# Kernel optimization log

Hardware: AMD Instinct MI355X
Metric: run time of the kernel (lower is better)

## Reference

```python
import math
import jax, jax.numpy as jnp
import numpy as np

B, S, HID, NH = 8, 512, 1024, 16
D = HID // NH          # head dim = 64
SPAN = 512             # att_span = max_relative_positions = max_position_embeddings


def _linear(x, W, b):
    # torch nn.Linear: y = x @ W.T + b, W is [out, in]
    return jnp.einsum('...i,oi->...o', x, W) + b


def _heads(x):
    # [B, S, HID] -> [B, NH, S, D]
    b, s, _ = x.shape
    return x.reshape(b, s, NH, D).transpose(0, 2, 1, 3)


def setup_inputs() -> dict:
    key = jax.random.key(0)
    ks = jax.random.split(key, 16)
    f = lambda i, shape, sc=1.0: jax.random.normal(ks[i], shape, dtype=jnp.float32) * sc
    return {
        'q': f(0, (B, S, HID)),
        'k': f(1, (B, S, HID)),
        'v': f(2, (B, S, HID)),
        'attention_mask': jnp.tril(jnp.ones((S, S), dtype=bool))[None, None],  # causal [1,1,S,S]
        'Wq': f(3, (HID, HID), 0.02), 'bq': jnp.zeros((HID,), jnp.float32),
        'Wk': f(4, (HID, HID), 0.02), 'bk': jnp.zeros((HID,), jnp.float32),
        'Wv': f(5, (HID, HID), 0.02), 'bv': jnp.zeros((HID,), jnp.float32),
        'Wpk': f(6, (HID, HID), 0.02), 'bpk': jnp.zeros((HID,), jnp.float32),
        'Wpq': f(7, (HID, HID), 0.02), 'bpq': jnp.zeros((HID,), jnp.float32),
        'rel_emb': f(8, (2 * SPAN, HID), 0.02),
    }


def reference(q, k, v, attention_mask, Wq, bq, Wk, bk, Wv, bv, Wpk, bpk, Wpq, bpq, rel_emb):
    scale_factor = 3  # 1 (content) + c2p + p2c
    scale = 1.0 / math.sqrt(D * scale_factor)

    ql = _heads(_linear(q, Wq, bq))   # [B,NH,S,D]
    kl = _heads(_linear(k, Wk, bk))
    vl = _heads(_linear(v, Wv, bv))

    # content-to-content scores
    scores = jnp.einsum('bhqd,bhkd->bhqk', ql, kl) * scale

    # relative positions (no bucketing since position_buckets = -1)
    rel = jnp.arange(S)[:, None] - jnp.arange(S)[None, :]          # [S,S]
    c2p_pos = jnp.clip(rel + SPAN, 0, 2 * SPAN - 1)
    p2c_pos = jnp.clip(-rel + SPAN, 0, 2 * SPAN - 1)

    # projected relative-position embeddings -> [NH, 2*SPAN, D]
    pk = _linear(rel_emb, Wpk, bpk).reshape(2 * SPAN, NH, D).transpose(1, 0, 2)
    pq = _linear(rel_emb, Wpq, bpq).reshape(2 * SPAN, NH, D).transpose(1, 0, 2)

    # content-to-position: out[b,h,q,k] = (q . pos_key)[b,h,q, c2p_pos[q,k]]
    c2p = jnp.einsum('bhqd,hjd->bhqj', ql, pk) * scale             # [B,NH,S,2*SPAN]
    c2p = jnp.take_along_axis(c2p, jnp.broadcast_to(c2p_pos[None, None], (B, NH, S, S)), axis=-1)

    # position-to-content: gathered[b,h,k,q] = (k . pos_query)[b,h,k, p2c_pos[k,q]], then transpose
    p2c = jnp.einsum('bhkd,hjd->bhkj', kl, pq) * scale             # [B,NH,S,2*SPAN]
    p2c = jnp.take_along_axis(p2c, jnp.broadcast_to(p2c_pos[None, None], (B, NH, S, S)), axis=-1)

    scores = scores + c2p + jnp.swapaxes(p2c, -1, -2)
    # subtract detached row max (as in torch: .max(...).values.detach())
    scores = scores - jax.lax.stop_gradient(scores.max(axis=-1, keepdims=True))

    # XSoftmax: masked softmax, then zero masked positions
    neg = jnp.float32(-1e30)
    probs = jax.nn.softmax(jnp.where(attention_mask, scores, neg), axis=-1)
    probs = jnp.where(attention_mask, probs, 0.0)

    ctx = jnp.einsum('bhqk,bhkd->bhqd', probs, vl)                 # [B,NH,S,D]
    return ctx.transpose(0, 2, 1, 3).reshape(B, S, HID)
```

## Files before the change

### kernel.cpp

```cpp
#include <hip/hip_runtime.h>
#include <hip/hip_bf16.h>
#include <math.h>

#define SCALE 0.07216878364870323f
#define NEG_BIG -1e30f

typedef __attribute__((ext_vector_type(8))) short bf16x8;
typedef __attribute__((ext_vector_type(4))) short bf16x4;
typedef __attribute__((ext_vector_type(4))) float f32x4;
#define MFMA_BF16 __builtin_amdgcn_mfma_f32_16x16x32_bf16

static __device__ __forceinline__ float bf2f(__hip_bfloat16 x) { return __bfloat162float(x); }
static __device__ __forceinline__ __hip_bfloat16 f2bf(float x) { return __float2bfloat16(x); }
static __device__ __forceinline__ short f2bs(float x) {
  union { __hip_bfloat16 b; short s; } u; u.b = __float2bfloat16(x); return u.s;
}
static __device__ __forceinline__ float s2f(short v) {
  union { float f; unsigned u; } x; x.u = ((unsigned)(unsigned short)v) << 16; return x.f;
}
static __device__ __forceinline__ bf16x4 cvt4(float4 f) {
  bf16x4 r; r[0] = f2bs(f.x); r[1] = f2bs(f.y); r[2] = f2bs(f.z); r[3] = f2bs(f.w);
  return r;
}
static __device__ __forceinline__ bf16x8 ldg8(const __hip_bfloat16* p) {
  return *(const bf16x8*)p;
}
static __device__ __forceinline__ void gl_lds16(const __hip_bfloat16* g, __hip_bfloat16* l) {
  __builtin_amdgcn_global_load_lds(
      (const __attribute__((address_space(1))) void*)g,
      (__attribute__((address_space(3))) void*)l, 16, 0, 0);
}

struct CvtJob { const float* src; __hip_bfloat16* dst; int n4; };
struct CvtArgs { CvtJob j[9]; };

__global__ __launch_bounds__(256) void cvt_kernel(CvtArgs a) {
  const CvtJob jb = a.j[blockIdx.y];
  const float4* s = (const float4*)jb.src;
  bf16x4* d = (bf16x4*)jb.dst;
  const int stride = gridDim.x * 256;
  for (int i = blockIdx.x * 256 + threadIdx.x; i < jb.n4; i += stride)
    d[i] = cvt4(s[i]);
}

struct Gemm { const __hip_bfloat16* A; const __hip_bfloat16* W;
              const float* bias; __hip_bfloat16* out; int mode; int mBits; int nBlk; };
struct ProjArgs { Gemm g[5]; };

__global__ __launch_bounds__(256) void proj_kernel(ProjArgs pa) {
  const Gemm g = pa.g[blockIdx.y];
  if ((int)blockIdx.x >= g.nBlk) return;
  __shared__ __hip_bfloat16 As[128][64];
  __shared__ __hip_bfloat16 Ws[128][64];

  const int bid = blockIdx.x;
  const int m0 = (bid & ((1 << g.mBits) - 1)) * 128;
  const int n0 = (bid >> g.mBits) * 128;
  const int tid = threadIdx.x;
  const int wave = tid >> 6, lane = tid & 63;
  const int q16 = lane >> 4, l16 = lane & 15;
  const int msub = (wave & 1) * 64, nsub = (wave >> 1) * 64;

  const int srow = wave * 32 + (lane >> 3);
  const int scol = (lane & 7) * 8;

  f32x4 acc[4][4] = {};

  for (int k0 = 0; k0 < 1024; k0 += 64) {
    __syncthreads();
#pragma unroll
    for (int c = 0; c < 4; c++) {
      gl_lds16(g.A + (size_t)(m0 + srow + c * 8) * 1024 + k0 + scol,
               &As[wave * 32 + c * 8][0]);
      gl_lds16(g.W + (size_t)(n0 + srow + c * 8) * 1024 + k0 + scol,
               &Ws[wave * 32 + c * 8][0]);
    }
    __syncthreads();
#pragma unroll
    for (int ki = 0; ki < 2; ki++) {
      const int ko = ki * 32 + q16 * 8;
      bf16x8 af[4];
#pragma unroll
      for (int mi = 0; mi < 4; mi++)
        af[mi] = *(const bf16x8*)(&As[msub + mi * 16 + l16][ko]);
#pragma unroll
      for (int ni = 0; ni < 4; ni++) {
        bf16x8 bw = *(const bf16x8*)(&Ws[nsub + ni * 16 + l16][ko]);
#pragma unroll
        for (int mi = 0; mi < 4; mi++)
          acc[mi][ni] = MFMA_BF16(af[mi], bw, acc[mi][ni], 0, 0, 0);
      }
    }
  }

  for (int ni = 0; ni < 4; ni++) {
    const int n = n0 + nsub + ni * 16 + l16;
    const int h = n >> 6, d = n & 63;
    const float bv = g.bias[n];
    for (int mi = 0; mi < 4; mi++) {
      const int mbase = m0 + msub + mi * 16 + q16 * 4;
      for (int rr = 0; rr < 4; rr++) {
        const int m = mbase + rr;
        const float val = acc[mi][ni][rr] + bv;
        size_t oidx;
        if (g.mode == 0) {
          const int b = m >> 9, s = m & 511;
          oidx = ((size_t)((b * 16 + h) * 512 + s)) * 64 + d;
        } else if (g.mode == 1) {
          const int b = m >> 9, s = m & 511;
          oidx = ((size_t)((b * 16 + h) * 64 + d)) * 512 + s;
        } else {
          oidx = ((size_t)(h * 512 + m)) * 64 + d;
        }
        g.out[oidx] = f2bf(val);
      }
    }
  }
}

__global__ __launch_bounds__(256) void attn_kernel(
    const __hip_bfloat16* __restrict__ ql,
    const __hip_bfloat16* __restrict__ kl,
    const __hip_bfloat16* __restrict__ vlT,
    const __hip_bfloat16* __restrict__ pk,
    const __hip_bfloat16* __restrict__ pq,
    float* __restrict__ out)
{
  __shared__ float rowsum[32];
  __shared__ __align__(16) __hip_bfloat16 sc[32][520];
  __shared__ __align__(16) __hip_bfloat16 ks_[32][72];
  __shared__ __align__(16) __hip_bfloat16 pks[32][72];
  __shared__ __align__(16) __hip_bfloat16 pqs[2][32][72];
  __shared__ __hip_bfloat16 cpb[2][32][34];
  __shared__ __align__(16) __hip_bfloat16 pqbT[2][2][32][36];

  const int bid = blockIdx.x;
  const int qt = 15 - (bid >> 7);
  const int bh = bid & 127;
  const int h = bh & 15, b = bh >> 4;
  const int q0 = qt * 32;

  const __hip_bfloat16* qlp = ql + (size_t)bh * 512 * 64;
  const __hip_bfloat16* klp = kl + (size_t)bh * 512 * 64;
  const __hip_bfloat16* vtp = vlT + (size_t)bh * 64 * 512;
  const __hip_bfloat16* pkp = pk + (size_t)h * 512 * 64;
  const __hip_bfloat16* pqp = pq + (size_t)h * 512 * 64;

  const int tid = threadIdx.x, wave = tid >> 6, lane = tid & 63;
  const int q16 = lane >> 4, l16 = lane & 15;
  const int wr = wave & 1, wc = wave >> 1;

  const int rowQ = q0 + wr * 16 + l16;
  bf16x8 aq0 = ldg8(qlp + (size_t)rowQ * 64 + q16 * 8);
  bf16x8 aq1 = ldg8(qlp + (size_t)rowQ * 64 + 32 + q16 * 8);

  {
    int4 z = {0, 0, 0, 0};
    *(int4*)(&pqs[1][tid >> 3][(tid & 7) * 8]) = z;
  }

  const int kEnd = q0 + 32;
  const int nIter = kEnd >> 5;

  const int sr = tid >> 3, sseg = tid & 7;
  int4 rKv, rPKv, rPQv;
  {
    rKv  = ((const int4*)(klp + (size_t)(q0 + sr) * 64))[sseg];
    rPKv = ((const int4*)(pkp + (size_t)(0 + sr) * 64))[sseg];
    rPQv = ((const int4*)(pqp + (size_t)(0 + sr) * 64))[sseg];
  }

  f32x4 qkPrev = {};
  int k0Prev = 0, parPrev = 0;

  for (int it = 0; it < nIter; ++it) {
    const int k0 = q0 - it * 32;
    const int par = it & 1;
    __syncthreads();
    *(int4*)(&ks_[sr][sseg * 8]) = rKv;
    *(int4*)(&pks[sr][sseg * 8]) = rPKv;
    *(int4*)(&pqs[par][sr][sseg * 8]) = rPQv;
    if (it > 0) {
#pragma unroll
      for (int rr = 0; rr < 4; rr++) {
        const int qh = wr * 16 + q16 * 4 + rr;
        const int kh = wc * 16 + l16;
        if (k0Prev + kh > q0 + qh) {
          sc[qh][k0Prev + kh] = f2bf(NEG_BIG);
        } else {
          const int dlt = qh - kh;
          const float c2pv = (dlt >= 0) ? bf2f(cpb[parPrev][qh][dlt])
                                        : bf2f(cpb[parPrev ^ 1][qh][dlt + 32]);
          const float p2cv = (dlt >= 0) ? bf2f(pqbT[parPrev][1][dlt][kh])
                                        : bf2f(pqbT[parPrev][0][dlt + 32][kh]);
          float v = (qkPrev[rr] + c2pv + p2cv) * SCALE;
          v = fminf(v, 60.f); v = fmaxf(v, -60.f);
          sc[qh][k0Prev + kh] = f2bf(v);
        }
      }
    }
    __syncthreads();
    if (it + 1 < nIter) {
      const int k0n = k0 - 32, jbn = q0 - k0n;
      rKv  = ((const int4*)(klp + (size_t)(k0n + sr) * 64))[sseg];
      rPKv = ((const int4*)(pkp + (size_t)(jbn + sr) * 64))[sseg];
      rPQv = ((const int4*)(pqp + (size_t)(jbn + sr) * 64))[sseg];
    }

    const int rA = wr * 16 + l16;
    const int rB = wc * 16 + l16;
    f32x4 qk = {}, cp = {}, p0 = {}, p1 = {};
#pragma unroll
    for (int ksi = 0; ksi < 2; ksi++) {
      const int ko = ksi * 32 + q16 * 8;
      bf16x8 aq = ksi ? aq1 : aq0;
      bf16x8 ak = *(const bf16x8*)(&ks_[rA][ko]);
      bf16x8 bk = *(const bf16x8*)(&ks_[rB][ko]);
      bf16x8 bp = *(const bf16x8*)(&pks[rB][ko]);
      bf16x8 b1 = *(const bf16x8*)(&pqs[par][rB][ko]);
      bf16x8 b0 = *(const bf16x8*)(&pqs[par ^ 1][rB][ko]);
      qk = MFMA_BF16(aq, bk, qk, 0, 0, 0);
      cp = MFMA_BF16(aq, bp, cp, 0, 0, 0);
      p0 = MFMA_BF16(ak, b0, p0, 0, 0, 0);
      p1 = MFMA_BF16(ak, b1, p1, 0, 0, 0);
    }
    {
      const int cw = wc * 16 + l16;
      const int rwb = wr * 16 + q16 * 4;
      bf16x4 v0, v1;
#pragma unroll
      for (int rr = 0; rr < 4; rr++) {
        cpb[par][rwb + rr][cw] = f2bf(cp[rr]);
        v0[rr] = f2bs(p0[rr]);
        v1[rr] = f2bs(p1[rr]);
      }
      *(bf16x4*)(&pqbT[par][0][cw][rwb]) = v0;
      *(bf16x4*)(&pqbT[par][1][cw][rwb]) = v1;
    }
    qkPrev = qk; k0Prev = k0; parPrev = par;
  }
  __syncthreads();
  {
#pragma unroll
    for (int rr = 0; rr < 4; rr++) {
      const int qh = wr * 16 + q16 * 4 + rr;
      const int kh = wc * 16 + l16;
      if (k0Prev + kh > q0 + qh) {
        sc[qh][k0Prev + kh] = f2bf(NEG_BIG);
      } else {
        const int dlt = qh - kh;
        const float c2pv = (dlt >= 0) ? bf2f(cpb[parPrev][qh][dlt])
                                      : bf2f(cpb[parPrev ^ 1][qh][dlt + 32]);
        const float p2cv = (dlt >= 0) ? bf2f(pqbT[parPrev][1][dlt][kh])
                                      : bf2f(pqbT[parPrev][0][dlt + 32][kh]);
        float v = (qkPrev[rr] + c2pv + p2cv) * SCALE;
        v = fminf(v, 60.f); v = fmaxf(v, -60.f);
        sc[qh][k0Prev + kh] = f2bf(v);
      }
    }
  }
  __syncthreads();

  {
    const int row = tid >> 3, sub = tid & 7;
    float m = NEG_BIG;
    for (int c = sub * 8; c < kEnd; c += 64) {
      bf16x8 x8 = *(const bf16x8*)(&sc[row][c]);
#pragma unroll
      for (int e = 0; e < 8; e++) m = fmaxf(m, s2f(x8[e]));
    }
    for (int off = 1; off < 8; off <<= 1) m = fmaxf(m, __shfl_xor(m, off));
    float s = 0.f;
    for (int c = sub * 8; c < kEnd; c += 64) {
      bf16x8 x8 = *(const bf16x8*)(&sc[row][c]);
      bf16x8 p8;
#pragma unroll
      for (int e = 0; e < 8; e++) {
        const float p = __expf(s2f(x8[e]) - m);
        p8[e] = f2bs(p);
        s += p;
      }
      *(bf16x8*)(&sc[row][c]) = p8;
    }
    for (int off = 1; off < 8; off <<= 1) s += __shfl_xor(s, off);
    if (sub == 0) rowsum[row] = s;
  }

  f32x4 octx[2] = {};
  __hip_bfloat16 (*vt)[72] = (__hip_bfloat16 (*)[72])(&pqs[0][0][0]);
  for (int k0 = 0; k0 < kEnd; k0 += 64) {
    __syncthreads();
    {
      const int r = tid >> 2, seg = tid & 3;
      const int4* src = (const int4*)(vtp + (size_t)r * 512 + k0);
      *(int4*)(&vt[r][seg * 8])       = src[seg];
      *(int4*)(&vt[r][(seg + 4) * 8]) = src[seg + 4];
    }
    __syncthreads();
#pragma unroll
    for (int sub = 0; sub < 2; sub++) {
      const int kk = k0 + sub * 32;
      if (kk < kEnd) {
        bf16x8 af = *(const bf16x8*)(&sc[wr * 16 + l16][kk + q16 * 8]);
#pragma unroll
        for (int cs = 0; cs < 2; cs++) {
          bf16x8 bv = *(const bf16x8*)(&vt[wc * 32 + cs * 16 + l16][sub * 32 + q16 * 8]);
          octx[cs] = MFMA_BF16(af, bv, octx[cs], 0, 0, 0);
        }
      }
    }
  }

  for (int cs = 0; cs < 2; cs++) {
    const int d = wc * 32 + cs * 16 + l16;
    for (int rr = 0; rr < 4; rr++) {
      const int qh = wr * 16 + q16 * 4 + rr;
      const float val = octx[cs][rr] / rowsum[qh];
      out[((size_t)(b * 512 + q0 + qh)) * 1024 + h * 64 + d] = val;
    }
  }
}

extern "C" void kernel_launch(void* const* d_in, const int* in_sizes, int n_in,
                              void* d_out, int out_size, void* d_ws, size_t ws_size,
                              hipStream_t stream) {
  const float* q   = (const float*)d_in[0];
  const float* k   = (const float*)d_in[1];
  const float* v   = (const float*)d_in[2];
  const float* Wq  = (const float*)d_in[4];
  const float* bq  = (const float*)d_in[5];
  const float* Wk  = (const float*)d_in[6];
  const float* bk  = (const float*)d_in[7];
  const float* Wv  = (const float*)d_in[8];
  const float* bv  = (const float*)d_in[9];
  const float* Wpk = (const float*)d_in[10];
  const float* bpk = (const float*)d_in[11];
  const float* Wpq = (const float*)d_in[12];
  const float* bpq = (const float*)d_in[13];
  const float* rel = (const float*)d_in[14];
  float* out = (float*)d_out;

  char* ws = (char*)d_ws;
  const size_t MB = 1u << 20;
  __hip_bfloat16* bqi  = (__hip_bfloat16*)(ws);
  __hip_bfloat16* bki  = (__hip_bfloat16*)(ws + 8 * MB);
  __hip_bfloat16* bvi  = (__hip_bfloat16*)(ws + 16 * MB);
  __hip_bfloat16* bWq  = (__hip_bfloat16*)(ws + 24 * MB);
  __hip_bfloat16* bWk  = (__hip_bfloat16*)(ws + 26 * MB);
  __hip_bfloat16* bWv  = (__hip_bfloat16*)(ws + 28 * MB);
  __hip_bfloat16* bWpk = (__hip_bfloat16*)(ws + 30 * MB);
  __hip_bfloat16* bWpq = (__hip_bfloat16*)(ws + 32 * MB);
  __hip_bfloat16* brel = (__hip_bfloat16*)(ws + 34 * MB);
  __hip_bfloat16* wql  = (__hip_bfloat16*)(ws + 35 * MB);
  __hip_bfloat16* wkl  = (__hip_bfloat16*)(ws + 43 * MB);
  __hip_bfloat16* wvlT = (__hip_bfloat16*)(ws + 51 * MB);
  __hip_bfloat16* wpk  = (__hip_bfloat16*)(ws + 59 * MB);
  __hip_bfloat16* wpq  = (__hip_bfloat16*)(ws + 60 * MB);

  CvtArgs ca;
  ca.j[0] = { q,   bqi,  4194304 / 4 };
  ca.j[1] = { k,   bki,  4194304 / 4 };
  ca.j[2] = { v,   bvi,  4194304 / 4 };
  ca.j[3] = { Wq,  bWq,  1048576 / 4 };
  ca.j[4] = { Wk,  bWk,  1048576 / 4 };
  ca.j[5] = { Wv,  bWv,  1048576 / 4 };
  ca.j[6] = { Wpk, bWpk, 1048576 / 4 };
  ca.j[7] = { Wpq, bWpq, 1048576 / 4 };
  ca.j[8] = { rel + (size_t)512 * 1024, brel, 524288 / 4 };
  cvt_kernel<<<dim3(1024, 9), 256, 0, stream>>>(ca);

  ProjArgs pj;
  pj.g[0] = { bqi,  bWq,  bq,  wql,  0, 5, 256 };
  pj.g[1] = { bki,  bWk,  bk,  wkl,  0, 5, 256 };
  pj.g[2] = { bvi,  bWv,  bv,  wvlT, 1, 5, 256 };
  pj.g[3] = { brel, bWpk, bpk, wpk,  2, 2, 32 };
  pj.g[4] = { brel, bWpq, bpq, wpq,  2, 2, 32 };
  proj_kernel<<<dim3(256, 5), 256, 0, stream>>>(pj);

  attn_kernel<<<2048, 256, 0, stream>>>(wql, wkl, wvlT, wpk, wpq, out);
}
```

Before: 248.0 us.

## Enlarge projection GEMM tiles to 256x256 with double-buffered swizzled LDS staging

Grows each projection GEMM block from 128x128 to a 256x256 output tile with 512 threads (8 waves), each wave computing 128x64. The global-to-LDS copies are double-buffered so the next K slice loads while the current one is multiplied. An XOR swizzle on the LDS column chunks is meant to cut bank conflicts. This raises per-block operand reuse and hides load latency, but leaves far fewer blocks (64 per big GEMM, 8 per small one), which risks underfilling the GPU's compute units, and it doubles LDS use per block.

```diff
diff --git a/kernel.cpp b/kernel.cpp
--- a/kernel.cpp
+++ b/kernel.cpp
@@ -47,58 +47,78 @@
               const float* bias; __hip_bfloat16* out; int mode; int mBits; int nBlk; };
 struct ProjArgs { Gemm g[5]; };
 
-__global__ __launch_bounds__(256) void proj_kernel(ProjArgs pa) {
+static __device__ __forceinline__ void stage256(const __hip_bfloat16* gbase,
+                                                __hip_bfloat16* lbase,
+                                                int wave, int lane) {
+  const int r = wave * 8 + (lane >> 3);
+  const int chunk = (lane & 7) ^ (lane >> 3);
+#pragma unroll
+  for (int c = 0; c < 4; c++) {
+    gl_lds16(gbase + (size_t)(c * 64 + r) * 1024 + chunk * 8,
+             lbase + (size_t)(c * 64 + wave * 8) * 64);
+  }
+}
+
+__global__ __launch_bounds__(512, 2) void proj_kernel(ProjArgs pa) {
   const Gemm g = pa.g[blockIdx.y];
   if ((int)blockIdx.x >= g.nBlk) return;
-  __shared__ __hip_bfloat16 As[128][64];
-  __shared__ __hip_bfloat16 Ws[128][64];
+  __shared__ __hip_bfloat16 As[2][256][64];
+  __shared__ __hip_bfloat16 Ws[2][256][64];
 
   const int bid = blockIdx.x;
-  const int m0 = (bid & ((1 << g.mBits) - 1)) * 128;
-  const int n0 = (bid >> g.mBits) * 128;
+  const int m0 = (bid & ((1 << g.mBits) - 1)) * 256;
+  const int n0 = (bid >> g.mBits) * 256;
   const int tid = threadIdx.x;
   const int wave = tid >> 6, lane = tid & 63;
   const int q16 = lane >> 4, l16 = lane & 15;
-  const int msub = (wave & 1) * 64, nsub = (wave >> 1) * 64;
-
-  const int srow = wave * 32 + (lane >> 3);
-  const int scol = (lane & 7) * 8;
-
-  f32x4 acc[4][4] = {};
-
-  for (int k0 = 0; k0 < 1024; k0 += 64) {
+  const int wr = wave >> 2, wc = wave & 3;
+
+  const __hip_bfloat16* Ag = g.A + (size_t)m0 * 1024;
+  const __hip_bfloat16* Wg = g.W + (size_t)n0 * 1024;
+
+  f32x4 acc[8][4] = {};
+
+  stage256(Ag, &As[0][0][0], wave, lane);
+  stage256(Wg, &Ws[0][0][0], wave, lane);
+
+  const int l7 = l16 & 7;
+
+  for (int t = 0; t < 16; ++t) {
+    const int cur = t & 1;
     __syncthreads();
-#pragma unroll
-    for (int c = 0; c < 4; c++) {
-      gl_lds16(g.A + (size_t)(m0 + srow + c * 8) * 1024 + k0 + scol,
-               &As[wave * 32 + c * 8][0]);
-      gl_lds16(g.W + (size_t)(n0 + srow + c * 8) * 1024 + k0 + scol,
-               &Ws[wave * 32 + c * 8][0]);
-    }
-    __syncthreads();
+    if (t + 1 < 16) {
+      const int k0n = (t + 1) * 64;
+      stage256(Ag + k0n, &As[cur ^ 1][0][0], wave, lane);
+      stage256(Wg + k0n, &Ws[cur ^ 1][0][0], wave, lane);
+    }
+    const __hip_bfloat16* Ac = &As[cur][0][0];
+    const __hip_bfloat16* Wc = &Ws[cur][0][0];
 #pragma unroll
     for (int ki = 0; ki < 2; ki++) {
-      const int ko = ki * 32 + q16 * 8;
-      bf16x8 af[4];
-#pragma unroll
-      for (int mi = 0; mi < 4; mi++)
-        af[mi] = *(const bf16x8*)(&As[msub + mi * 16 + l16][ko]);
+      const int csw = ((ki * 4 + q16) ^ l7) * 8;
+      bf16x8 af[8];
+#pragma unroll
+      for (int mi = 0; mi < 8; mi++)
+        af[mi] = *(const bf16x8*)(Ac + (size_t)(wr * 128 + mi * 16 + l16) * 64 + csw);
 #pragma unroll
       for (int ni = 0; ni < 4; ni++) {
-        bf16x8 bw = *(const bf16x8*)(&Ws[nsub + ni * 16 + l16][ko]);
-#pragma unroll
-        for (int mi = 0; mi < 4; mi++)
+        bf16x8 bw = *(const bf16x8*)(Wc + (size_t)(wc * 64 + ni * 16 + l16) * 64 + csw);
+#pragma unroll
+        for (int mi = 0; mi < 8; mi++)
           acc[mi][ni] = MFMA_BF16(af[mi], bw, acc[mi][ni], 0, 0, 0);
       }
     }
   }
 
+#pragma unroll
   for (int ni = 0; ni < 4; ni++) {
-    const int n = n0 + nsub + ni * 16 + l16;
+    const int n = n0 + wc * 64 + ni * 16 + l16;
     const int h = n >> 6, d = n & 63;
     const float bv = g.bias[n];
-    for (int mi = 0; mi < 4; mi++) {
-      const int mbase = m0 + msub + mi * 16 + q16 * 4;
+#pragma unroll
+    for (int mi = 0; mi < 8; mi++) {
+      const int mbase = m0 + wr * 128 + mi * 16 + q16 * 4;
+#pragma unroll
       for (int rr = 0; rr < 4; rr++) {
         const int m = mbase + rr;
         const float val = acc[mi][ni][rr] + bv;
@@ -370,12 +390,12 @@
   cvt_kernel<<<dim3(1024, 9), 256, 0, stream>>>(ca);
 
   ProjArgs pj;
-  pj.g[0] = { bqi,  bWq,  bq,  wql,  0, 5, 256 };
-  pj.g[1] = { bki,  bWk,  bk,  wkl,  0, 5, 256 };
-  pj.g[2] = { bvi,  bWv,  bv,  wvlT, 1, 5, 256 };
-  pj.g[3] = { brel, bWpk, bpk, wpk,  2, 2, 32 };
-  pj.g[4] = { brel, bWpq, bpq, wpq,  2, 2, 32 };
-  proj_kernel<<<dim3(256, 5), 256, 0, stream>>>(pj);
+  pj.g[0] = { bqi,  bWq,  bq,  wql,  0, 4, 64 };
+  pj.g[1] = { bki,  bWk,  bk,  wkl,  0, 4, 64 };
+  pj.g[2] = { bvi,  bWv,  bv,  wvlT, 1, 4, 64 };
+  pj.g[3] = { brel, bWpk, bpk, wpk,  2, 1, 8 };
+  pj.g[4] = { brel, bWpq, bpq, wpq,  2, 1, 8 };
+  proj_kernel<<<dim3(64, 5), 512, 0, stream>>>(pj);
 
   attn_kernel<<<2048, 256, 0, stream>>>(wql, wkl, wvlT, wpk, wpq, out);
 }
```

After: 248.8 us. Within noise of the previous version (+0.3%).
